# Optimization experiments

Measured on AMD Instinct MI355X. Metric: run time of the kernel, lower is better.

The kernel has to match this reference:

```python
import jax, jax.numpy as jnp
import numpy as np

EMB = 32      # emb_size = input_size // 2
IN = 64       # input_size
H = 128       # hidden_size
OUT = 256     # output_size (byte vocab)
TEMP = 1e-3   # Decoder_lstm.temperature


def _bytes(x):
    # x: [N] nonneg int32 -> [N, 4] big-endian bytes (vectorized get_bytes_2d)
    shifts = jnp.array([24, 16, 8, 0], dtype=x.dtype)
    return (x[:, None] >> shifts) & 0xFF


def _embed4(tables, byts):
    # tables: [4, 256, EMB]; byts: [N, 4] -> [N, 4*EMB] (concat of 4 gathers)
    return jnp.concatenate([tables[i][byts[:, i]] for i in range(4)], axis=-1)


def _encoder(x, W, b):
    # Encoder: sigmoid(Linear(4*EMB -> EMB))
    return jax.nn.sigmoid(x @ W.T + b)


def _lstm(xs, h0, c0, W_ih, W_hh, b_ih, b_hh):
    # xs: [S, B, IN]; PyTorch gate order i, f, g, o
    def step(carry, x_t):
        h, c = carry
        g = x_t @ W_ih.T + b_ih + h @ W_hh.T + b_hh  # [B, 4H]
        i, f, gg, o = jnp.split(g, 4, axis=-1)
        c = jax.nn.sigmoid(f) * c + jax.nn.sigmoid(i) * jnp.tanh(gg)
        h = jax.nn.sigmoid(o) * jnp.tanh(c)
        return (h, c), None
    (hf, cf), _ = jax.lax.scan(step, (h0, c0), xs)
    return hf, cf


def reference(inp, h0, c0, pc_emb, addr_emb, enc_W, enc_b, W_ih, W_hh, b_ih, b_hh, dec_W, dec_b, fc1_W, fc1_b, fc2_W, fc2_b):
    b, s, _ = inp.shape
    pc = inp[:, :, 0].reshape(-1)
    ad = inp[:, :, 1].reshape(-1)
    # byte decomposition + embedding gather + TimeDistributed encoder MLP
    pc_e = _encoder(_embed4(pc_emb, _bytes(pc)), enc_W, enc_b).reshape(b, s, EMB)
    ad_e = _encoder(_embed4(addr_emb, _bytes(ad)), enc_W, enc_b).reshape(b, s, EMB)
    emb = jnp.concatenate([pc_e, ad_e], axis=-1)  # [b, s, IN]
    # deterministic surrogate for KDE sample mean (expected value of 200 KDE draws)
    dist = jnp.mean(emb, axis=1)  # [b, IN]
    hf, _ = _lstm(jnp.swapaxes(emb, 0, 1), h0[0], c0[0], W_ih, W_hh, b_ih, b_hh)
    h_n = hf[None]  # [1, b, H] == hidden_cell[0]
    # Decoder_lstm: 4 parallel linears + low-temperature softmax
    logits = jnp.einsum('xbh,koh->kxbo', h_n, dec_W) + dec_b[:, None, None, :]  # [4,1,b,OUT]
    probs = jax.nn.softmax(logits / TEMP, axis=-1)
    # get_freq_rec: probs @ embedding tables, encoder MLP, concat dist, small MLP
    be = jnp.einsum('kxbo,koe->xbke', probs, addr_emb).reshape(1, b, 4 * EMB)
    fe = _encoder(be, enc_W, enc_b)[0]  # [b, EMB]
    fr_in = jnp.concatenate([fe, dist], axis=-1)  # [b, 3*EMB]
    fr = jax.nn.sigmoid(jax.nn.relu(fr_in @ fc1_W.T + fc1_b) @ fc2_W.T + fc2_b)
    return probs, logits, fr[:, 0], fr[:, 1]


def setup_inputs() -> dict:
    ks = jax.random.split(jax.random.key(0), 18)
    B, S = 64, 2048
    g = lambda k, shp: 0.1 * jax.random.normal(k, shp, dtype=jnp.float32)
    return {
        'inp': jax.random.randint(ks[0], (B, S, 2), 0, 2147483647, dtype=jnp.int32),
        'h0': g(ks[1], (1, B, H)),
        'c0': g(ks[2], (1, B, H)),
        'pc_emb': g(ks[3], (4, 256, EMB)),
        'addr_emb': g(ks[4], (4, 256, EMB)),
        'enc_W': g(ks[5], (EMB, 4 * EMB)),
        'enc_b': g(ks[6], (EMB,)),
        'W_ih': g(ks[7], (4 * H, IN)),
        'W_hh': g(ks[8], (4 * H, H)),
        'b_ih': g(ks[9], (4 * H,)),
        'b_hh': g(ks[10], (4 * H,)),
        'dec_W': g(ks[11], (4, OUT, H)),
        'dec_b': g(ks[12], (4, OUT)),
        'fc1_W': g(ks[13], (10, 3 * EMB)),
        'fc1_b': g(ks[14], (10,)),
        'fc2_W': g(ks[15], (2, 10)),
        'fc2_b': g(ks[16], (2,)),
    }
```

## Files before the change

### kernel.cpp

```cpp
#include <hip/hip_runtime.h>
#include <math.h>
#include <stdint.h>

#define EMBS 32
#define INS 64
#define HS 128
#define OUTS 256
#define BS 64
#define SS 2048

typedef _Float16 half2v __attribute__((ext_vector_type(2)));

static constexpr size_t WS_DIST  = (size_t)BS * SS * INS;
static constexpr size_t WS_HFIN  = WS_DIST + (size_t)BS * INS;
static constexpr size_t WS_XW    = WS_HFIN + (size_t)BS * HS;
static constexpr size_t WS_SMALL = WS_XW;
static constexpr size_t WS_BIG   = WS_XW + (size_t)BS * SS * 256;

__device__ __forceinline__ float fexp2(float x) {
#if __has_builtin(__builtin_amdgcn_exp2f)
    return __builtin_amdgcn_exp2f(x);
#else
    return exp2f(x);
#endif
}
__device__ __forceinline__ float frcp(float x) {
#if __has_builtin(__builtin_amdgcn_rcpf)
    return __builtin_amdgcn_rcpf(x);
#else
    return 1.f / x;
#endif
}
__device__ __forceinline__ float sigm(float x)  { return frcp(1.f + fexp2(-1.44269504f * x)); }
__device__ __forceinline__ float ftanh(float x) { return 1.f - 2.f * frcp(1.f + fexp2(2.88539008f * x)); }

__device__ __forceinline__ float fdot2f(half2v a, half2v b, float c) {
#if __has_builtin(__builtin_amdgcn_fdot2)
    return __builtin_amdgcn_fdot2(a, b, c, false);
#else
    return c + (float)a.x * (float)b.x + (float)a.y * (float)b.y;
#endif
}

__device__ __forceinline__ half2v pack2(float a, float b) {
    half2v r; r.x = (_Float16)a; r.y = (_Float16)b; return r;
}

__device__ __forceinline__ void gate_map(int tid, int& u, bool& lo, int& g0, int& g1) {
    int l = tid & 63;
    u = ((tid >> 6) << 5) + (l & 31);
    lo = (l < 32);
    g0 = lo ? u : 128 + u;
    g1 = lo ? 256 + u : 384 + u;
}

__global__ __launch_bounds__(256) void k_embed(
    const int* __restrict__ inp, const float* __restrict__ pc_emb,
    const float* __restrict__ ad_emb, const float* __restrict__ encW,
    const float* __restrict__ encB, float* __restrict__ emb)
{
    int idx = blockIdx.x * 256 + threadIdx.x;
    int b = idx >> 11, t = idx & 2047;
    size_t base = (size_t)b * SS + t;
    int2 pa = ((const int2*)inp)[base];
    float* outp = emb + base * INS;

    float in[128];
    #pragma unroll
    for (int st = 0; st < 2; st++) {
        int v = (st == 0) ? pa.x : pa.y;
        const float* tbl = (st == 0) ? pc_emb : ad_emb;
        #pragma unroll
        for (int i = 0; i < 4; i++) {
            int by = (v >> (24 - 8 * i)) & 255;
            const float4* row = (const float4*)(tbl + ((size_t)i * 256 + by) * EMBS);
            #pragma unroll
            for (int k = 0; k < 8; k++) {
                float4 f = row[k];
                in[i * 32 + k * 4 + 0] = f.x;
                in[i * 32 + k * 4 + 1] = f.y;
                in[i * 32 + k * 4 + 2] = f.z;
                in[i * 32 + k * 4 + 3] = f.w;
            }
        }
        for (int e = 0; e < EMBS; e++) {
            const float* w = encW + e * 128;
            float acc = encB[e];
            #pragma unroll
            for (int k = 0; k < 128; k++) acc += in[k] * w[k];
            outp[st * EMBS + e] = sigm(acc);
        }
    }
}

__global__ __launch_bounds__(256) void k_dist(const float* __restrict__ emb,
                                              float* __restrict__ dist)
{
    int b = blockIdx.x;
    int j = threadIdx.x & 63;
    int grp = threadIdx.x >> 6;
    float s = 0.f;
    for (int t = grp; t < SS; t += 4) s += emb[((size_t)b * SS + t) * INS + j];
    __shared__ float red[4][64];
    red[grp][j] = s;
    __syncthreads();
    if (grp == 0)
        dist[b * 64 + j] = (red[0][j] + red[1][j] + red[2][j] + red[3][j]) * (1.f / SS);
}

#define XW_ROWS 64
__global__ __launch_bounds__(256) void k_xw(
    const float* __restrict__ emb, const float* __restrict__ Wih,
    const float* __restrict__ bih, const float* __restrict__ bhh,
    half2v* __restrict__ xwv)
{
    int tid = threadIdx.x;
    size_t r0 = (size_t)blockIdx.x * XW_ROWS;
    int u, g0, g1; bool lo;
    gate_map(tid, u, lo, g0, g1);

    half2v wa[32], wb[32];
    const float* pa_ = Wih + (size_t)g0 * INS;
    const float* pb_ = Wih + (size_t)g1 * INS;
    #pragma unroll
    for (int i = 0; i < 32; i++) {
        wa[i] = pack2(pa_[2 * i], pa_[2 * i + 1]);
        wb[i] = pack2(pb_[2 * i], pb_[2 * i + 1]);
    }
    float ba = bih[g0] + bhh[g0], bb = bih[g1] + bhh[g1];

    __shared__ alignas(16) half2v xsh[XW_ROWS * 32];
    const float4* src = (const float4*)(emb + r0 * INS);
    #pragma unroll
    for (int k = 0; k < 4; k++) {
        int fi = k * 256 + tid;
        float4 v = src[fi];
        xsh[fi * 2]     = pack2(v.x, v.y);
        xsh[fi * 2 + 1] = pack2(v.z, v.w);
    }
    __syncthreads();

    #pragma unroll 2
    for (int r = 0; r < XW_ROWS; r++) {
        const half2v* xr = &xsh[r * 32];
        float a0 = 0.f, a1 = 0.f, b0 = 0.f, b1 = 0.f;
        #pragma unroll
        for (int i = 0; i < 32; i += 2) {
            half2v x0 = xr[i], x1 = xr[i + 1];
            a0 = fdot2f(x0, wa[i], a0);
            a1 = fdot2f(x1, wa[i + 1], a1);
            b0 = fdot2f(x0, wb[i], b0);
            b1 = fdot2f(x1, wb[i + 1], b1);
        }
        xwv[(r0 + r) * 256 + tid] = pack2(ba + a0 + a1, bb + b0 + b1);
    }
}

__global__ __launch_bounds__(256, 1) void k_lstm4(
    const half2v* __restrict__ xw, const float* __restrict__ h0,
    const float* __restrict__ c0, const float* __restrict__ Whh,
    float* __restrict__ hfin)
{
    int b = blockIdx.x;
    int tid = threadIdx.x;
    int u, g0, g1; bool lo;
    gate_map(tid, u, lo, g0, g1);

    half2v wh0[64], wh1[64];
    const float* h0p = Whh + (size_t)g0 * HS;
    const float* h1p = Whh + (size_t)g1 * HS;
    #pragma unroll
    for (int i = 0; i < 64; i++) {
        wh0[i] = pack2(h0p[2 * i], h0p[2 * i + 1]);
        wh1[i] = pack2(h1p[2 * i], h1p[2 * i + 1]);
    }

    __shared__ alignas(16) _Float16 hsh[2][HS];
    float c = 0.f, h = 0.f;
    if (!lo) c = c0[b * HS + u];
    if (tid < 128) hsh[0][tid] = (_Float16)h0[b * HS + tid];
    __syncthreads();

    const half2v* xwrow = xw + (size_t)b * SS * 256 + tid;
    half2v x0 = xwrow[0];
    half2v x1 = xwrow[256];
    half2v x2 = xwrow[512];
    half2v x3 = xwrow[768];

    int p = 0;
    for (int t = 0; t < SS; t++) {
        int tn = (t + 4 < SS) ? (t + 4) : (SS - 1);
        half2v xn = xwrow[(size_t)tn * 256];

        const half2v* hr = (const half2v*)hsh[p];
        float a0a = 0.f, a0b = 0.f, a1a = 0.f, a1b = 0.f;
        #pragma unroll
        for (int i = 0; i < 64; i += 2) {
            half2v h0v = hr[i], h1v = hr[i + 1];
            a0a = fdot2f(h0v, wh0[i], a0a);
            a0b = fdot2f(h1v, wh0[i + 1], a0b);
            a1a = fdot2f(h0v, wh1[i], a1a);
            a1b = fdot2f(h1v, wh1[i + 1], a1b);
        }
        float a0 = (float)x0.x + a0a + a0b;
        float a1 = (float)x0.y + a1a + a1b;

        float act0 = sigm(a0);
        float act1 = lo ? ftanh(a1) : sigm(a1);
        float ig = act0 * act1;
        float pig = __shfl_xor(ig, 32, 64);

        if (!lo) {
            c = __builtin_fmaf(act0, c, pig);
            h = act1 * ftanh(c);
            hsh[p ^ 1][u] = (_Float16)h;
        }

        asm volatile("s_waitcnt lgkmcnt(0)" ::: "memory");
        __builtin_amdgcn_s_barrier();
        __builtin_amdgcn_sched_barrier(0);

        p ^= 1;
        x0 = x1; x1 = x2; x2 = x3; x3 = xn;
    }
    if (!lo) hfin[b * HS + u] = h;
}

__global__ __launch_bounds__(256, 1) void k_lstm_fb(
    const float* __restrict__ emb, const float* __restrict__ h0,
    const float* __restrict__ c0, const float* __restrict__ Wih,
    const float* __restrict__ Whh, const float* __restrict__ bih,
    const float* __restrict__ bhh, float* __restrict__ hfin)
{
    int b = blockIdx.x;
    int tid = threadIdx.x;

    half2v wih[2][32], whh[2][64];
    #pragma unroll
    for (int g = 0; g < 2; g++) {
        int gg = tid + g * 256;
        const float* wr = Wih + (size_t)gg * INS;
        #pragma unroll
        for (int i = 0; i < 32; i++) wih[g][i] = pack2(wr[2 * i], wr[2 * i + 1]);
        const float* hr = Whh + (size_t)gg * HS;
        #pragma unroll
        for (int i = 0; i < 64; i++) whh[g][i] = pack2(hr[2 * i], hr[2 * i + 1]);
    }
    float bias0 = bih[tid] + bhh[tid];
    float bias1 = bih[tid + 256] + bhh[tid + 256];

    __shared__ alignas(16) half2v xh[96];
    __shared__ float f_act[128], o_act[128];
    __shared__ float xf[64], hf[128];

    float c = 0.f, h = 0.f;
    if (tid < 128) c = c0[b * HS + tid];

    const float* xrow = emb + (size_t)b * SS * INS;
    if (tid < 64) xf[tid] = xrow[tid];
    if (tid < 128) hf[tid] = h0[b * HS + tid];
    __syncthreads();
    if (tid < 32) xh[tid] = pack2(xf[2 * tid], xf[2 * tid + 1]);
    else if (tid < 96) { int uu = tid - 32; xh[tid] = pack2(hf[2 * uu], hf[2 * uu + 1]); }
    __syncthreads();

    for (int t = 0; t < SS; t++) {
        float xn = 0.f;
        if (tid >= 128 && tid < 192 && t + 1 < SS) xn = xrow[(size_t)(t + 1) * INS + (tid - 128)];

        float a0a = 0.f, a0b = 0.f, a1a = 0.f, a1b = 0.f;
        #pragma unroll
        for (int i = 0; i < 32; i += 2) {
            half2v x0 = xh[i], x1 = xh[i + 1];
            a0a = fdot2f(x0, wih[0][i], a0a);
            a0b = fdot2f(x1, wih[0][i + 1], a0b);
            a1a = fdot2f(x0, wih[1][i], a1a);
            a1b = fdot2f(x1, wih[1][i + 1], a1b);
        }
        #pragma unroll
        for (int i = 0; i < 64; i += 2) {
            half2v h0v = xh[32 + i], h1v = xh[32 + i + 1];
            a0a = fdot2f(h0v, whh[0][i], a0a);
            a0b = fdot2f(h1v, whh[0][i + 1], a0b);
            a1a = fdot2f(h0v, whh[1][i], a1a);
            a1b = fdot2f(h1v, whh[1][i + 1], a1b);
        }
        float a0 = bias0 + a0a + a0b;
        float a1 = bias1 + a1a + a1b;

        float iact = 0.f, gact = 0.f;
        if (tid < 128) { iact = sigm(a0); gact = ftanh(a1); }
        else           { f_act[tid - 128] = sigm(a0); o_act[tid - 128] = sigm(a1); }
        __syncthreads();

        if (tid < 128) {
            c = f_act[tid] * c + iact * gact;
            h = o_act[tid] * ftanh(c);
            hf[tid] = h;
        } else if (tid < 192) {
            xf[tid - 128] = xn;
        }
        __syncthreads();

        if (tid < 32) xh[tid] = pack2(xf[2 * tid], xf[2 * tid + 1]);
        else if (tid < 96) { int uu = tid - 32; xh[tid] = pack2(hf[2 * uu], hf[2 * uu + 1]); }
        __syncthreads();
    }
    if (tid < 128) hfin[b * HS + tid] = h;
}

__global__ __launch_bounds__(256) void k_head(
    const float* __restrict__ hfin, const float* __restrict__ decW,
    const float* __restrict__ decB, const float* __restrict__ ad_emb,
    const float* __restrict__ encW, const float* __restrict__ encB,
    const float* __restrict__ dist, const float* __restrict__ fc1W,
    const float* __restrict__ fc1b, const float* __restrict__ fc2W,
    const float* __restrict__ fc2b, float* __restrict__ outp)
{
    int b = blockIdx.x;
    int tid = threadIdx.x;
    __shared__ float hsh[128];
    __shared__ float logit_s[4][256];
    __shared__ float probs_s[4][256];
    __shared__ float be_s[128];
    __shared__ float fe_dist[96];
    __shared__ float fr1[10];

    if (tid < 128) hsh[tid] = hfin[b * HS + tid];
    __syncthreads();

    #pragma unroll
    for (int k = 0; k < 4; k++) {
        const float* w = decW + ((size_t)k * OUTS + tid) * HS;
        float acc = decB[k * OUTS + tid];
        #pragma unroll 8
        for (int hh = 0; hh < HS; hh++) acc += hsh[hh] * w[hh];
        logit_s[k][tid] = acc;
        outp[65536 + k * 16384 + b * 256 + tid] = acc;
    }
    __syncthreads();

    {
        int k = tid >> 6, lane = tid & 63;
        float v0 = logit_s[k][lane],       v1 = logit_s[k][lane + 64];
        float v2 = logit_s[k][lane + 128], v3 = logit_s[k][lane + 192];
        float m = fmaxf(fmaxf(v0, v1), fmaxf(v2, v3));
        for (int off = 32; off; off >>= 1) m = fmaxf(m, __shfl_xor(m, off, 64));
        float e0 = fexp2((v0 - m) * 1442.695041f), e1 = fexp2((v1 - m) * 1442.695041f);
        float e2 = fexp2((v2 - m) * 1442.695041f), e3 = fexp2((v3 - m) * 1442.695041f);
        float s = e0 + e1 + e2 + e3;
        for (int off = 32; off; off >>= 1) s += __shfl_xor(s, off, 64);
        float inv = 1.f / s;
        float p0 = e0 * inv, p1 = e1 * inv, p2 = e2 * inv, p3 = e3 * inv;
        probs_s[k][lane] = p0;        probs_s[k][lane + 64] = p1;
        probs_s[k][lane + 128] = p2;  probs_s[k][lane + 192] = p3;
        outp[k * 16384 + b * 256 + lane] = p0;
        outp[k * 16384 + b * 256 + lane + 64] = p1;
        outp[k * 16384 + b * 256 + lane + 128] = p2;
        outp[k * 16384 + b * 256 + lane + 192] = p3;
    }
    __syncthreads();

    if (tid < 128) {
        int k = tid >> 5, e = tid & 31;
        const float* te = ad_emb + (size_t)k * OUTS * EMBS + e;
        float acc = 0.f;
        #pragma unroll 8
        for (int o = 0; o < OUTS; o++) acc += probs_s[k][o] * te[o * EMBS];
        be_s[tid] = acc;
    }
    __syncthreads();

    if (tid < 32) {
        const float* w = encW + tid * 128;
        float acc = encB[tid];
        #pragma unroll 8
        for (int kk = 0; kk < 128; kk++) acc += be_s[kk] * w[kk];
        fe_dist[tid] = sigm(acc);
    } else if (tid < 96) {
        fe_dist[tid] = dist[b * 64 + (tid - 32)];
    }
    __syncthreads();

    if (tid < 10) {
        float acc = fc1b[tid];
        for (int kk = 0; kk < 96; kk++) acc += fe_dist[kk] * fc1W[tid * 96 + kk];
        fr1[tid] = fmaxf(acc, 0.f);
    }
    __syncthreads();

    if (tid < 2) {
        float acc = fc2b[tid];
        for (int kk = 0; kk < 10; kk++) acc += fr1[kk] * fc2W[tid * 10 + kk];
        outp[131072 + tid * 64 + b] = sigm(acc);
    }
}

extern "C" void kernel_launch(void* const* d_in, const int* in_sizes, int n_in,
                              void* d_out, int out_size, void* d_ws, size_t ws_size,
                              hipStream_t stream)
{
    const int*   inp    = (const int*)d_in[0];
    const float* h0     = (const float*)d_in[1];
    const float* c0     = (const float*)d_in[2];
    const float* pc_emb = (const float*)d_in[3];
    const float* ad_emb = (const float*)d_in[4];
    const float* encW   = (const float*)d_in[5];
    const float* encB   = (const float*)d_in[6];
    const float* Wih    = (const float*)d_in[7];
    const float* Whh    = (const float*)d_in[8];
    const float* bih    = (const float*)d_in[9];
    const float* bhh    = (const float*)d_in[10];
    const float* decW   = (const float*)d_in[11];
    const float* decB   = (const float*)d_in[12];
    const float* fc1W   = (const float*)d_in[13];
    const float* fc1b   = (const float*)d_in[14];
    const float* fc2W   = (const float*)d_in[15];
    const float* fc2b   = (const float*)d_in[16];

    if (ws_size < WS_SMALL * 4ull) return;

    float* ws   = (float*)d_ws;
    float* emb  = ws;
    float* dist = ws + WS_DIST;
    float* hfin = ws + WS_HFIN;
    float* outp = (float*)d_out;
    bool big = (ws_size >= WS_BIG * 4ull);

    hipLaunchKernelGGL(k_embed, dim3(512), dim3(256), 0, stream,
                       inp, pc_emb, ad_emb, encW, encB, emb);
    hipLaunchKernelGGL(k_dist, dim3(64), dim3(256), 0, stream, emb, dist);
    if (big) {
        half2v* xwv = (half2v*)(ws + WS_XW);
        hipLaunchKernelGGL(k_xw, dim3(BS * SS / XW_ROWS), dim3(256), 0, stream,
                           emb, Wih, bih, bhh, xwv);
        hipLaunchKernelGGL(k_lstm4, dim3(64), dim3(256), 0, stream,
                           xwv, h0, c0, Whh, hfin);
    } else {
        hipLaunchKernelGGL(k_lstm_fb, dim3(64), dim3(256), 0, stream,
                           emb, h0, c0, Wih, Whh, bih, bhh, hfin);
    }
    hipLaunchKernelGGL(k_head, dim3(64), dim3(256), 0, stream,
                       hfin, decW, decB, ad_emb, encW, encB, dist,
                       fc1W, fc1b, fc2W, fc2b, outp);
}
```

Before: 1.582 ms.

## Split LSTM recurrent matvec over K halves across paired lanes

Each thread now holds weights for all four gates of its unit but only over half of the hidden dimension (64 of 128). The two halves are combined with cross-half shuffles, where the old scheme gave each thread two full gate rows. Each thread's LDS reads of h drop to half per step, which is meant to shorten the per-step critical path of the serial recurrence. The time loop is also unrolled by four with static buffer indices and prefetch registers. In exchange, each step pays two extra shuffles, and combining the gates may introduce ordering or precision differences.

```diff
diff --git a/kernel.cpp b/kernel.cpp
--- a/kernel.cpp
+++ b/kernel.cpp
@@ -156,23 +156,31 @@
     }
 }
 
-__global__ __launch_bounds__(256, 1) void k_lstm4(
+__global__ __launch_bounds__(256, 1) void k_lstm6(
     const half2v* __restrict__ xw, const float* __restrict__ h0,
     const float* __restrict__ c0, const float* __restrict__ Whh,
     float* __restrict__ hfin)
 {
     int b = blockIdx.x;
     int tid = threadIdx.x;
-    int u, g0, g1; bool lo;
-    gate_map(tid, u, lo, g0, g1);
-
-    half2v wh0[64], wh1[64];
-    const float* h0p = Whh + (size_t)g0 * HS;
-    const float* h1p = Whh + (size_t)g1 * HS;
-    #pragma unroll
-    for (int i = 0; i < 64; i++) {
-        wh0[i] = pack2(h0p[2 * i], h0p[2 * i + 1]);
-        wh1[i] = pack2(h1p[2 * i], h1p[2 * i + 1]);
+    int u, g0_, g1_; bool lo;
+    gate_map(tid, u, lo, g0_, g1_);
+    int koff = lo ? 0 : 64;
+    int kv   = lo ? 0 : 32;
+
+    half2v wI[32], wF[32], wG[32], wO[32];
+    {
+        const float* rI = Whh + (size_t)(u)       * HS + koff;
+        const float* rF = Whh + (size_t)(128 + u) * HS + koff;
+        const float* rG = Whh + (size_t)(256 + u) * HS + koff;
+        const float* rO = Whh + (size_t)(384 + u) * HS + koff;
+        #pragma unroll
+        for (int i = 0; i < 32; i++) {
+            wI[i] = pack2(rI[2 * i], rI[2 * i + 1]);
+            wF[i] = pack2(rF[2 * i], rF[2 * i + 1]);
+            wG[i] = pack2(rG[2 * i], rG[2 * i + 1]);
+            wO[i] = pack2(rO[2 * i], rO[2 * i + 1]);
+        }
     }
 
     __shared__ alignas(16) _Float16 hsh[2][HS];
@@ -182,47 +190,56 @@
     __syncthreads();
 
     const half2v* xwrow = xw + (size_t)b * SS * 256 + tid;
-    half2v x0 = xwrow[0];
-    half2v x1 = xwrow[256];
-    half2v x2 = xwrow[512];
-    half2v x3 = xwrow[768];
-
-    int p = 0;
-    for (int t = 0; t < SS; t++) {
-        int tn = (t + 4 < SS) ? (t + 4) : (SS - 1);
-        half2v xn = xwrow[(size_t)tn * 256];
-
-        const half2v* hr = (const half2v*)hsh[p];
-        float a0a = 0.f, a0b = 0.f, a1a = 0.f, a1b = 0.f;
-        #pragma unroll
-        for (int i = 0; i < 64; i += 2) {
-            half2v h0v = hr[i], h1v = hr[i + 1];
-            a0a = fdot2f(h0v, wh0[i], a0a);
-            a0b = fdot2f(h1v, wh0[i + 1], a0b);
-            a1a = fdot2f(h0v, wh1[i], a1a);
-            a1b = fdot2f(h1v, wh1[i + 1], a1b);
-        }
-        float a0 = (float)x0.x + a0a + a0b;
-        float a1 = (float)x0.y + a1a + a1b;
-
-        float act0 = sigm(a0);
-        float act1 = lo ? ftanh(a1) : sigm(a1);
-        float ig = act0 * act1;
-        float pig = __shfl_xor(ig, 32, 64);
-
-        if (!lo) {
-            c = __builtin_fmaf(act0, c, pig);
-            h = act1 * ftanh(c);
-            hsh[p ^ 1][u] = (_Float16)h;
-        }
-
-        asm volatile("s_waitcnt lgkmcnt(0)" ::: "memory");
-        __builtin_amdgcn_s_barrier();
-        __builtin_amdgcn_sched_barrier(0);
-
-        p ^= 1;
-        x0 = x1; x1 = x2; x2 = x3; x3 = xn;
-    }
+    half2v xb0 = xwrow[0];
+    half2v xb1 = xwrow[256];
+    half2v xb2 = xwrow[512];
+    half2v xb3 = xwrow[768];
+
+#define LSTEP(XB, RB, TN)                                                      \
+    {                                                                          \
+        const half2v* hb = (const half2v*)hsh[RB] + kv;                        \
+        half2v hr[32];                                                         \
+        _Pragma("unroll")                                                      \
+        for (int j_ = 0; j_ < 32; j_++) hr[j_] = hb[j_];                       \
+        float pI = 0.f, pF = 0.f, pG = 0.f, pO = 0.f;                          \
+        _Pragma("unroll")                                                      \
+        for (int j_ = 0; j_ < 32; j_++) {                                      \
+            half2v hv = hr[j_];                                                \
+            pI = fdot2f(hv, wI[j_], pI);                                       \
+            pF = fdot2f(hv, wF[j_], pF);                                       \
+            pG = fdot2f(hv, wG[j_], pG);                                       \
+            pO = fdot2f(hv, wO[j_], pO);                                       \
+        }                                                                      \
+                \
+        float r1 = __shfl_xor(lo ? pF : pI, 32, 64); \
+        float r2 = __shfl_xor(lo ? pO : pG, 32, 64); \
+        float pre0 = (lo ? pI : pF) + r1 + (float)XB.x;                        \
+        float pre1 = (lo ? pG : pO) + r2 + (float)XB.y;                        \
+        float act0 = sigm(pre0);                            \
+        float act1 = lo ? ftanh(pre1) : sigm(pre1);         \
+        float pig = __shfl_xor(act0 * act1, 32, 64);      \
+        if (!lo) {                                                             \
+            c = __builtin_fmaf(act0, c, pig);                                  \
+            h = act1 * ftanh(c);                                               \
+            hsh[RB ^ 1][u] = (_Float16)h;                                      \
+        }                                                                      \
+        {                                                                      \
+            int tn_ = (TN) < SS ? (TN) : (SS - 1);                             \
+            XB = xwrow[(size_t)tn_ * 256];                                     \
+        }                                                                      \
+        asm volatile("s_waitcnt lgkmcnt(0)" ::: "memory");                     \
+        __builtin_amdgcn_s_barrier();                                          \
+        __builtin_amdgcn_sched_barrier(0);                                     \
+    }
+
+    for (int t = 0; t < SS; t += 4) {
+        LSTEP(xb0, 0, t + 4)
+        LSTEP(xb1, 1, t + 5)
+        LSTEP(xb2, 0, t + 6)
+        LSTEP(xb3, 1, t + 7)
+    }
+#undef LSTEP
+
     if (!lo) hfin[b * HS + u] = h;
 }
 
@@ -434,7 +451,7 @@
         half2v* xwv = (half2v*)(ws + WS_XW);
         hipLaunchKernelGGL(k_xw, dim3(BS * SS / XW_ROWS), dim3(256), 0, stream,
                            emb, Wih, bih, bhh, xwv);
-        hipLaunchKernelGGL(k_lstm4, dim3(64), dim3(256), 0, stream,
+        hipLaunchKernelGGL(k_lstm6, dim3(64), dim3(256), 0, stream,
                            xwv, h0, c0, Whh, hfin);
     } else {
         hipLaunchKernelGGL(k_lstm_fb, dim3(64), dim3(256), 0, stream,
```

Measured after the change: 1.497 ms. 1.06x faster.
